# Performance work log

Hardware: AMD Instinct MI355X
Metric: run time of the kernel (lower is better)

## Reference

```python
import jax, jax.numpy as jnp
import numpy as np

N = 8192        # nodes
E = 262144      # edges (avg degree 32)
IN_CH = 256
CH = 128
SLOPE = 0.2     # PyG GATv2Conv default negative_slope


def gatv2(x, src, dst, wl, wr, att, b):
    """Single-head GATv2Conv (PyG defaults: share_weights=False, self-loops
    already appended to src/dst). x: [N, in]; wl, wr: [out, in]; att: [out]."""
    xl = x @ wl.T                      # [N, out] source-side transform (x_j)
    xr = x @ wr.T                      # [N, out] target-side transform (x_i)
    # per-edge attention logit: att . LeakyReLU(x_l[src] + x_r[dst])
    e = jax.nn.leaky_relu(xl[src] + xr[dst], SLOPE) @ att   # [E']
    # segment softmax over incoming edges of each target node
    m = jax.ops.segment_max(e, dst, num_segments=N)
    p = jnp.exp(e - m[dst])
    s = jax.ops.segment_sum(p, dst, num_segments=N)
    alpha = p / s[dst]                 # every node has a self-loop -> s > 0
    out = jax.ops.segment_sum(alpha[:, None] * xl[src], dst, num_segments=N)
    return out + b


def setup_inputs() -> dict:
    key = jax.random.key(0)
    ks = jax.random.split(key, 2 + 5 * 3)
    inp = {
        "x": jax.random.normal(ks[0], (N, IN_CH), dtype=jnp.float32),
        "edge_index": jax.random.randint(ks[1], (2, E), 0, N, dtype=jnp.int64),
    }
    dims = [(CH, IN_CH), (2 * CH, CH), (CH, 2 * CH), (CH, 2 * CH), (IN_CH, CH)]
    ki = 2
    for i, (oc, ic) in enumerate(dims, start=1):
        sc = (2.0 / (ic + oc)) ** 0.5  # glorot-ish
        inp[f"w{i}l"] = jax.random.normal(ks[ki], (oc, ic), dtype=jnp.float32) * sc
        inp[f"w{i}r"] = jax.random.normal(ks[ki + 1], (oc, ic), dtype=jnp.float32) * sc
        inp[f"a{i}"] = jax.random.normal(ks[ki + 2], (oc,), dtype=jnp.float32) * sc
        inp[f"b{i}"] = jnp.zeros((oc,), dtype=jnp.float32)
        ki += 3
    return inp


def reference(x, edge_index,
              w1l, w1r, a1, b1,
              w2l, w2r, a2, b2,
              w3l, w3r, a3, b3,
              w4l, w4r, a4, b4,
              w5l, w5r, a5, b5):
    loops = jnp.arange(N, dtype=edge_index.dtype)
    src = jnp.concatenate([edge_index[0], loops])   # add_self_loops=True
    dst = jnp.concatenate([edge_index[1], loops])
    h = jax.nn.relu(gatv2(x, src, dst, w1l, w1r, a1, b1))          # [N, CH]
    z = jax.nn.relu(gatv2(h, src, dst, w2l, w2r, a2, b2))          # [N, 2CH]
    re = jax.nn.relu(gatv2(z, src, dst, w3l, w3r, a3, b3))         # [N, CH]
    recon_edge = jax.nn.sigmoid(re @ re.T)                         # [N, N]
    xd = jax.nn.relu(gatv2(z, src, dst, w4l, w4r, a4, b4))         # [N, CH]
    x_rec = jax.nn.relu(gatv2(xd, src, dst, w5l, w5r, a5, b5))     # [N, IN_CH]
    return recon_edge, x_rec, z
```

## Files before the change

kernel.cpp:

```cpp
#include <hip/hip_runtime.h>
#include <hip/hip_bf16.h>
#include <math.h>

#define N_NODES 8192
#define N_EDGES 262144
#define EP (N_EDGES + N_NODES)
#define SLOPE 0.2f

typedef short bf16x8 __attribute__((ext_vector_type(8)));
typedef short short4v __attribute__((ext_vector_type(4)));
typedef float f32x4 __attribute__((ext_vector_type(4)));

__global__ void detect_i64(const int* __restrict__ raw, int* __restrict__ flag) {
    if (threadIdx.x == 0 && blockIdx.x == 0) {
        int acc = 0;
        for (int i = 0; i < 64; ++i) acc |= raw[2 * i + 1];
        *flag = (acc == 0) ? 1 : 0;
    }
}

__global__ void extract_hist(const int* __restrict__ raw, const int* __restrict__ flag,
                             int* __restrict__ esrc, int* __restrict__ edst,
                             int* __restrict__ counts) {
    int k = blockIdx.x * blockDim.x + threadIdx.x;
    if (k >= N_EDGES) return;
    int s, d;
    if (*flag) {
        s = raw[2 * (size_t)k];
        d = raw[2 * ((size_t)N_EDGES + k)];
    } else {
        s = raw[k];
        d = raw[N_EDGES + k];
    }
    esrc[k] = s;
    edst[k] = d;
    atomicAdd(&counts[d], 1);
}

__global__ void scan_k(const int* __restrict__ counts, int* __restrict__ row_ptr) {
    __shared__ int part[256];
    int t = threadIdx.x;
    int base = t * 32;
    int loc[32];
    int s = 0;
    for (int i = 0; i < 32; ++i) { loc[i] = s; s += counts[base + i] + 1; }
    part[t] = s;
    __syncthreads();
    for (int off = 1; off < 256; off <<= 1) {
        int tmp = (t >= off) ? part[t - off] : 0;
        __syncthreads();
        part[t] += tmp;
        __syncthreads();
    }
    int incl = part[t];
    int excl = incl - s;
    for (int i = 0; i < 32; ++i) row_ptr[base + i] = excl + loc[i];
    if (t == 255) row_ptr[N_NODES] = incl;
}

__global__ void scatter_k(const int* __restrict__ esrc, const int* __restrict__ edst,
                          const int* __restrict__ row_ptr, int* __restrict__ cursor,
                          int* __restrict__ ssrc) {
    int k = blockIdx.x * blockDim.x + threadIdx.x;
    if (k >= EP) return;
    int s, d;
    if (k < N_EDGES) { s = esrc[k]; d = edst[k]; }
    else             { s = d = k - N_EDGES; }
    int pos = row_ptr[d] + atomicAdd(&cursor[d], 1);
    ssrc[pos] = s;
}

__global__ void split3(const float* __restrict__ in, short* __restrict__ out, int logK) {
    int K = 1 << logK;
    int total = (N_NODES << logK) >> 2;
    int i = blockIdx.x * blockDim.x + threadIdx.x;
    if (i >= total) return;
    int r = i >> (logK - 2);
    int c4 = (i & ((1 << (logK - 2)) - 1)) << 2;
    f32x4 a = *(const f32x4*)&in[((size_t)r << logK) + c4];
    short4v h4, l4;
#pragma unroll
    for (int j = 0; j < 4; ++j) {
        __hip_bfloat16 hb = __float2bfloat16(a[j]);
        float hf = __bfloat162float(hb);
        __hip_bfloat16 lb = __float2bfloat16(a[j] - hf);
        h4[j] = *(short*)&hb;
        l4[j] = *(short*)&lb;
    }
    size_t ro = (size_t)r * (3 << logK);
    *(short4v*)&out[ro + c4] = h4;
    *(short4v*)&out[ro + K + c4] = l4;
    *(short4v*)&out[ro + 2 * K + c4] = h4;
}

struct WPrep {
    const float* wl[5];
    const float* wr[5];
    int oc[5];
    int lk[5];
};

__global__ void prep_w3_all(WPrep P, short* __restrict__ out) {
    int gid = blockIdx.x * blockDim.x + threadIdx.x;
    int l = gid >> 16;
    if (l >= 5) return;
    int rem = gid & 65535;
    int lk = P.lk[l], K = 1 << lk;
    int r = rem >> lk, c = rem & (K - 1);
    int OC = P.oc[l];
    const float* w = (r < OC) ? P.wl[l] : P.wr[l];
    int rr = (r < OC) ? r : r - OC;
    float a = w[((size_t)rr << lk) + c];
    __hip_bfloat16 hb = __float2bfloat16(a);
    float hf = __bfloat162float(hb);
    __hip_bfloat16 lb = __float2bfloat16(a - hf);
    short hs = *(short*)&hb, lo = *(short*)&lb;
    size_t ro = (size_t)l * 196608 + (size_t)r * 3 * K;
    out[ro + c] = hs;
    out[ro + K + c] = hs;
    out[ro + 2 * K + c] = lo;
}

#if __has_builtin(__builtin_amdgcn_global_load_lds)
#define GL16(gsrc, lbase, lofs)                                                       \
    __builtin_amdgcn_global_load_lds((const __attribute__((address_space(1))) void*)(gsrc), \
                                     (__attribute__((address_space(3))) void*)(lbase), 16, 0, 0)
#else
#define GL16(gsrc, lbase, lofs) (*(bf16x8*)((lbase) + (lofs)) = *(const bf16x8*)(gsrc))
#endif

__global__ __launch_bounds__(256) void gemm_bf16_nt(const short* __restrict__ A3,
                                                    const short* __restrict__ W3,
                                                    float* __restrict__ XL,
                                                    float* __restrict__ XR,
                                                    int K3, int N2, int OC) {
    __shared__ __align__(16) short As[2][4096];
    __shared__ __align__(16) short Bs[2][4096];
    int tid = threadIdx.x;
    int gx = gridDim.x;
    int lgx = (gx == 8) ? 3 : 2;
    int orig = blockIdx.x + (blockIdx.y << lgx);
    int nwg = gx << 7;
    int swzb = (orig & 7) * (nwg >> 3) + (orig >> 3);
    int bx = swzb & (gx - 1), by = swzb >> lgx;
    int i0 = by * 64, j0 = bx * 64;

    int wave = tid >> 6, lane = tid & 63;
    int b0 = wave * 1024 + lane * 16;
    int row0 = b0 >> 7;
    int rb0 = b0 & 127;
    int scb = rb0 ^ ((row0 & 7) << 4);
    const short* gA0 = A3 + (size_t)(i0 + row0) * K3 + (scb >> 1);
    const short* gA1 = A3 + (size_t)(i0 + row0 + 32) * K3 + (scb >> 1);
    const short* gB0 = W3 + (size_t)(j0 + row0) * K3 + (scb >> 1);
    const short* gB1 = W3 + (size_t)(j0 + row0 + 32) * K3 + (scb >> 1);
    int lofs = lane * 8;

#define STAGE(pb, k0s)                                      \
    do {                                                    \
        GL16(gA0 + (k0s), &As[pb][wave * 512], lofs);       \
        GL16(gA1 + (k0s), &As[pb][2048 + wave * 512], lofs);\
        GL16(gB0 + (k0s), &Bs[pb][wave * 512], lofs);       \
        GL16(gB1 + (k0s), &Bs[pb][2048 + wave * 512], lofs);\
    } while (0)

    int wr = (wave >> 1) * 32, wc = (wave & 1) * 32;
    int lm = lane & 15, quad = lane >> 4;
    f32x4 acc[2][2] = {};
    int nt = K3 >> 6;
    STAGE(0, 0);
    int cur = 0;
    for (int t = 0; t < nt; ++t) {
        if (t + 1 < nt) {
            STAGE(cur ^ 1, (t + 1) << 6);
            asm volatile("s_waitcnt vmcnt(4)" ::: "memory");
        } else {
            asm volatile("s_waitcnt vmcnt(0)" ::: "memory");
        }
        __builtin_amdgcn_s_barrier();
        __builtin_amdgcn_sched_barrier(0);
        const char* Ab = (const char*)&As[cur][0];
        const char* Bb = (const char*)&Bs[cur][0];
#pragma unroll
        for (int ks = 0; ks < 2; ++ks) {
            int kb = ks * 64 + quad * 16;
            bf16x8 a[2], b[2];
#pragma unroll
            for (int u = 0; u < 2; ++u) {
                int r = wr + u * 16 + lm;
                a[u] = *(const bf16x8*)(Ab + (((r << 7) | kb) ^ ((r & 7) << 4)));
            }
#pragma unroll
            for (int v = 0; v < 2; ++v) {
                int r = wc + v * 16 + lm;
                b[v] = *(const bf16x8*)(Bb + (((r << 7) | kb) ^ ((r & 7) << 4)));
            }
#pragma unroll
            for (int u = 0; u < 2; ++u)
#pragma unroll
                for (int v = 0; v < 2; ++v)
                    acc[u][v] = __builtin_amdgcn_mfma_f32_16x16x32_bf16(a[u], b[v], acc[u][v], 0, 0, 0);
        }
        __builtin_amdgcn_sched_barrier(0);
        __builtin_amdgcn_s_barrier();
        cur ^= 1;
    }
#undef STAGE
    float* Cb;
    int col0;
    if (j0 < OC) { Cb = XL; col0 = j0; } else { Cb = XR; col0 = j0 - OC; }
#pragma unroll
    for (int u = 0; u < 2; ++u)
#pragma unroll
        for (int v = 0; v < 2; ++v)
#pragma unroll
            for (int r = 0; r < 4; ++r) {
                int row = i0 + wr + u * 16 + quad * 4 + r;
                int col = col0 + wc + v * 16 + lm;
                Cb[(size_t)row * OC + col] = acc[u][v][r];
            }
}

#define LSTR 136

__global__ __launch_bounds__(256) void recon_mfma(const unsigned short* __restrict__ Rb,
                                                  float* __restrict__ C) {
    __shared__ __align__(16) short As[128 * LSTR];
    __shared__ __align__(16) short Bs[128 * LSTR];
    int tid = threadIdx.x;
    int orig = blockIdx.x + blockIdx.y * 64;
    int swzb = (orig & 7) * 512 + (orig >> 3);
    int bx = swzb & 63, by = swzb >> 6;
    int i0 = by * 128, j0 = bx * 128;
    const short* R = (const short*)Rb;
#pragma unroll
    for (int c = 0; c < 8; ++c) {
        int idx = tid + c * 256;
        int row = idx >> 4, col = (idx & 15) * 8;
        *(bf16x8*)(&As[row * LSTR + col]) = *(const bf16x8*)(&R[(size_t)(i0 + row) * 128 + col]);
        *(bf16x8*)(&Bs[row * LSTR + col]) = *(const bf16x8*)(&R[(size_t)(j0 + row) * 128 + col]);
    }
    __syncthreads();
    int wave = tid >> 6, lane = tid & 63;
    int wr = (wave >> 1) * 64, wc = (wave & 1) * 64;
    int lm = lane & 15, quad = lane >> 4;
    f32x4 acc[4][4] = {};
#pragma unroll
    for (int ks = 0; ks < 4; ++ks) {
        int ko = ks * 32 + quad * 8;
        bf16x8 a[4], b[4];
#pragma unroll
        for (int u = 0; u < 4; ++u)
            a[u] = *(const bf16x8*)(&As[(wr + u * 16 + lm) * LSTR + ko]);
#pragma unroll
        for (int v = 0; v < 4; ++v)
            b[v] = *(const bf16x8*)(&Bs[(wc + v * 16 + lm) * LSTR + ko]);
#pragma unroll
        for (int u = 0; u < 4; ++u)
#pragma unroll
            for (int v = 0; v < 4; ++v)
                acc[u][v] = __builtin_amdgcn_mfma_f32_16x16x32_bf16(a[u], b[v], acc[u][v], 0, 0, 0);
    }
#pragma unroll
    for (int u = 0; u < 4; ++u)
#pragma unroll
        for (int v = 0; v < 4; ++v)
#pragma unroll
            for (int r = 0; r < 4; ++r) {
                int row = i0 + wr + u * 16 + quad * 4 + r;
                int col = j0 + wc + v * 16 + lm;
                float val = acc[u][v][r];
                C[(size_t)row * 8192 + col] = 1.0f / (1.0f + __expf(-val));
            }
}

__global__ __launch_bounds__(256) void gat_node256(const int* __restrict__ row_ptr,
                                                   const int* __restrict__ ssrc,
                                                   const float* __restrict__ XL,
                                                   const float* __restrict__ XR,
                                                   const float* __restrict__ att,
                                                   const float* __restrict__ bias,
                                                   float* __restrict__ outf,
                                                   short* __restrict__ a3) {
    __shared__ float sacc[4][256];
    __shared__ float sm[4], ss[4];
    int d = blockIdx.x, t = threadIdx.x;
    int lane = t & 63, wave = t >> 6;
    int beg = row_ptr[d], end = row_ptr[d + 1];
    f32x4 xr = *(const f32x4*)&XR[(size_t)d * 256 + lane * 4];
    f32x4 at = *(const f32x4*)&att[lane * 4];
    float m = -INFINITY, s = 0.0f;
    f32x4 acc = {0.0f, 0.0f, 0.0f, 0.0f};
    for (int p = beg + wave; p < end; p += 4) {
        int si = ssrc[p];
        f32x4 v = *(const f32x4*)&XL[(size_t)si * 256 + lane * 4];
        float e = 0.0f;
#pragma unroll
        for (int j = 0; j < 4; ++j) {
            float u = v[j] + xr[j];
            u = (u > 0.0f) ? u : SLOPE * u;
            e += u * at[j];
        }
#pragma unroll
        for (int off = 32; off; off >>= 1) e += __shfl_xor(e, off, 64);
        float mn = fmaxf(m, e);
        float f = __expf(m - mn), p0 = __expf(e - mn);
        s = s * f + p0;
#pragma unroll
        for (int j = 0; j < 4; ++j) acc[j] = acc[j] * f + p0 * v[j];
        m = mn;
    }
    *(f32x4*)&sacc[wave][lane * 4] = acc;
    if (lane == 0) { sm[wave] = m; ss[wave] = s; }
    __syncthreads();
    float M = fmaxf(fmaxf(sm[0], sm[1]), fmaxf(sm[2], sm[3]));
    float tot = 0.0f, st = 0.0f;
#pragma unroll
    for (int w = 0; w < 4; ++w) {
        float fw = __expf(sm[w] - M);
        tot += sacc[w][t] * fw;
        st += ss[w] * fw;
    }
    float val = fmaxf(tot / st + bias[t], 0.0f);
    if (outf) outf[(size_t)d * 256 + t] = val;
    if (a3) {
        __hip_bfloat16 hb = __float2bfloat16(val);
        float hf = __bfloat162float(hb);
        __hip_bfloat16 lb = __float2bfloat16(val - hf);
        size_t ro = (size_t)d * 768;
        a3[ro + t] = *(short*)&hb;
        a3[ro + 256 + t] = *(short*)&lb;
        a3[ro + 512 + t] = *(short*)&hb;
    }
}

__global__ __launch_bounds__(256) void gat_node128(const int* __restrict__ row_ptr,
                                                   const int* __restrict__ ssrc,
                                                   const float* __restrict__ XL,
                                                   const float* __restrict__ XR,
                                                   const float* __restrict__ att,
                                                   const float* __restrict__ bias,
                                                   float* __restrict__ outf,
                                                   short* __restrict__ a3,
                                                   unsigned short* __restrict__ rb) {
    __shared__ float sacc[8][128];
    __shared__ float sm[8], ss[8];
    int d = blockIdx.x, t = threadIdx.x;
    int ln = t & 31, hw = t >> 5;
    int beg = row_ptr[d], end = row_ptr[d + 1];
    f32x4 xr = *(const f32x4*)&XR[(size_t)d * 128 + ln * 4];
    f32x4 at = *(const f32x4*)&att[ln * 4];
    float m = -INFINITY, s = 0.0f;
    f32x4 acc = {0.0f, 0.0f, 0.0f, 0.0f};
    for (int p = beg + hw; p < end; p += 8) {
        int si = ssrc[p];
        f32x4 v = *(const f32x4*)&XL[(size_t)si * 128 + ln * 4];
        float e = 0.0f;
#pragma unroll
        for (int j = 0; j < 4; ++j) {
            float u = v[j] + xr[j];
            u = (u > 0.0f) ? u : SLOPE * u;
            e += u * at[j];
        }
#pragma unroll
        for (int off = 16; off; off >>= 1) e += __shfl_xor(e, off, 32);
        float mn = fmaxf(m, e);
        float f = __expf(m - mn), p0 = __expf(e - mn);
        s = s * f + p0;
#pragma unroll
        for (int j = 0; j < 4; ++j) acc[j] = acc[j] * f + p0 * v[j];
        m = mn;
    }
    *(f32x4*)&sacc[hw][ln * 4] = acc;
    if (ln == 0) { sm[hw] = m; ss[hw] = s; }
    __syncthreads();
    if (t < 128) {
        float M = sm[0];
#pragma unroll
        for (int w = 1; w < 8; ++w) M = fmaxf(M, sm[w]);
        float tot = 0.0f, st = 0.0f;
#pragma unroll
        for (int w = 0; w < 8; ++w) {
            float fw = __expf(sm[w] - M);
            tot += sacc[w][t] * fw;
            st += ss[w] * fw;
        }
        float val = fmaxf(tot / st + bias[t], 0.0f);
        if (outf) outf[(size_t)d * 128 + t] = val;
        if (a3) {
            __hip_bfloat16 hb = __float2bfloat16(val);
            float hf = __bfloat162float(hb);
            __hip_bfloat16 lb = __float2bfloat16(val - hf);
            size_t ro = (size_t)d * 384;
            a3[ro + t] = *(short*)&hb;
            a3[ro + 128 + t] = *(short*)&lb;
            a3[ro + 256 + t] = *(short*)&hb;
        }
        if (rb) {
            __hip_bfloat16 hb = __float2bfloat16(val);
            rb[d * 128 + t] = *(unsigned short*)&hb;
        }
    }
}

static inline int ceil_div(int a, int b) { return (a + b - 1) / b; }

extern "C" void kernel_launch(void* const* d_in, const int* in_sizes, int n_in,
                              void* d_out, int out_size, void* d_ws, size_t ws_size,
                              hipStream_t stream) {
    const float* x    = (const float*)d_in[0];
    const int*   eraw = (const int*)d_in[1];

    WPrep P;
    const float* att[5];
    const float* bia[5];
    for (int l = 0; l < 5; ++l) {
        P.wl[l] = (const float*)d_in[2 + 4 * l + 0];
        P.wr[l] = (const float*)d_in[2 + 4 * l + 1];
        att[l]  = (const float*)d_in[2 + 4 * l + 2];
        bia[l]  = (const float*)d_in[2 + 4 * l + 3];
    }
    const int och[5]  = {128, 256, 128, 128, 256};
    const int logK[5] = {8, 7, 8, 8, 7};
    for (int l = 0; l < 5; ++l) { P.oc[l] = och[l]; P.lk[l] = logK[l]; }

    float* outp  = (float*)d_out;
    float* recon = outp;
    float* xrec  = outp + (size_t)67108864;
    float* zout  = outp + (size_t)69206016;

    float* W = (float*)d_ws;
    float* XL    = W;
    float* XR    = W + 2097152;
    short* A3    = (short*)(W + 4194304);
    short* W3all = (short*)(W + 7340032);
    unsigned short* Rb = (unsigned short*)(W + 7831552);
    int* I       = (int*)(W + 8355840);
    int* counts  = I;
    int* cursor  = I + 8192;
    int* row_ptr = I + 16384;
    int* ssrc    = I + 24577;
    int* esrc    = I + 294913;
    int* edst    = I + 557057;
    int* flag    = I + 819201;

    hipMemsetAsync(counts, 0, 2 * 8192 * sizeof(int), stream);
    detect_i64<<<1, 64, 0, stream>>>(eraw, flag);
    extract_hist<<<ceil_div(N_EDGES, 256), 256, 0, stream>>>(eraw, flag, esrc, edst, counts);
    scan_k<<<1, 256, 0, stream>>>(counts, row_ptr);
    scatter_k<<<ceil_div(EP, 256), 256, 0, stream>>>(esrc, edst, row_ptr, cursor, ssrc);

    prep_w3_all<<<1280, 256, 0, stream>>>(P, W3all);
    split3<<<ceil_div(N_NODES * 256 / 4, 256), 256, 0, stream>>>(x, A3, 8);

    for (int l = 0; l < 5; ++l) {
        int lk = logK[l], OC = och[l];
        int N2 = OC << 1, K3 = 3 << lk;

        dim3 g(N2 / 64, N_NODES / 64);
        gemm_bf16_nt<<<g, 256, 0, stream>>>(A3, W3all + (size_t)l * 196608, XL, XR, K3, N2, OC);

        if (OC == 128) {
            float* of = nullptr;
            short* a3 = (l == 0 || l == 3) ? A3 : nullptr;
            unsigned short* rb = (l == 2) ? Rb : nullptr;
            gat_node128<<<N_NODES, 256, 0, stream>>>(row_ptr, ssrc, XL, XR, att[l], bia[l], of, a3, rb);
        } else {
            float* of = (l == 1) ? zout : xrec;
            short* a3 = (l == 1) ? A3 : nullptr;
            gat_node256<<<N_NODES, 256, 0, stream>>>(row_ptr, ssrc, XL, XR, att[l], bia[l], of, a3);
        }

        if (l == 2) {
            dim3 gr(64, 64);
            recon_mfma<<<gr, 256, 0, stream>>>(Rb, recon);
        }
    }
}
```

Baseline: 596.2 us.

## Exploit recon symmetry, unroll GAT edge loops, fuse prep and detect kernels

The recon kernel now computes only upper-triangular 128x128 tiles (2080 blocks instead of 4096) and writes each off-diagonal tile twice, the second time transposed through LDS. This roughly halves the MFMA and sigmoid work while keeping the full 256MB output write. The GAT node kernels handle two edges per iteration to expose more memory-level parallelism. The int64 detection kernel is folded into extract_hist, and the x split and weight prep kernels are merged into one launch to cut launch overhead. The transposed write path adds LDS traffic and an extra sync.

```diff
diff --git a/kernel.cpp b/kernel.cpp
--- a/kernel.cpp
+++ b/kernel.cpp
@@ -11,21 +11,21 @@
 typedef short short4v __attribute__((ext_vector_type(4)));
 typedef float f32x4 __attribute__((ext_vector_type(4)));
 
-__global__ void detect_i64(const int* __restrict__ raw, int* __restrict__ flag) {
-    if (threadIdx.x == 0 && blockIdx.x == 0) {
-        int acc = 0;
-        for (int i = 0; i < 64; ++i) acc |= raw[2 * i + 1];
-        *flag = (acc == 0) ? 1 : 0;
-    }
-}
-
-__global__ void extract_hist(const int* __restrict__ raw, const int* __restrict__ flag,
+__global__ void extract_hist(const int* __restrict__ raw,
                              int* __restrict__ esrc, int* __restrict__ edst,
                              int* __restrict__ counts) {
-    int k = blockIdx.x * blockDim.x + threadIdx.x;
+    __shared__ int sflag;
+    int t = threadIdx.x;
+    if (t < 64) {
+        unsigned long long b = __ballot(raw[2 * t + 1] != 0);
+        if (t == 0) sflag = (b == 0ULL) ? 1 : 0;
+    }
+    __syncthreads();
+    int i64f = sflag;
+    int k = blockIdx.x * blockDim.x + t;
     if (k >= N_EDGES) return;
     int s, d;
-    if (*flag) {
+    if (i64f) {
         s = raw[2 * (size_t)k];
         d = raw[2 * ((size_t)N_EDGES + k)];
     } else {
@@ -70,29 +70,6 @@
     ssrc[pos] = s;
 }
 
-__global__ void split3(const float* __restrict__ in, short* __restrict__ out, int logK) {
-    int K = 1 << logK;
-    int total = (N_NODES << logK) >> 2;
-    int i = blockIdx.x * blockDim.x + threadIdx.x;
-    if (i >= total) return;
-    int r = i >> (logK - 2);
-    int c4 = (i & ((1 << (logK - 2)) - 1)) << 2;
-    f32x4 a = *(const f32x4*)&in[((size_t)r << logK) + c4];
-    short4v h4, l4;
-#pragma unroll
-    for (int j = 0; j < 4; ++j) {
-        __hip_bfloat16 hb = __float2bfloat16(a[j]);
-        float hf = __bfloat162float(hb);
-        __hip_bfloat16 lb = __float2bfloat16(a[j] - hf);
-        h4[j] = *(short*)&hb;
-        l4[j] = *(short*)&lb;
-    }
-    size_t ro = (size_t)r * (3 << logK);
-    *(short4v*)&out[ro + c4] = h4;
-    *(short4v*)&out[ro + K + c4] = l4;
-    *(short4v*)&out[ro + 2 * K + c4] = h4;
-}
-
 struct WPrep {
     const float* wl[5];
     const float* wr[5];
@@ -100,25 +77,45 @@
     int lk[5];
 };
 
-__global__ void prep_w3_all(WPrep P, short* __restrict__ out) {
+__global__ void prep_all(WPrep P, const float* __restrict__ x,
+                         short* __restrict__ W3all, short* __restrict__ A3) {
     int gid = blockIdx.x * blockDim.x + threadIdx.x;
-    int l = gid >> 16;
-    if (l >= 5) return;
-    int rem = gid & 65535;
-    int lk = P.lk[l], K = 1 << lk;
-    int r = rem >> lk, c = rem & (K - 1);
-    int OC = P.oc[l];
-    const float* w = (r < OC) ? P.wl[l] : P.wr[l];
-    int rr = (r < OC) ? r : r - OC;
-    float a = w[((size_t)rr << lk) + c];
-    __hip_bfloat16 hb = __float2bfloat16(a);
-    float hf = __bfloat162float(hb);
-    __hip_bfloat16 lb = __float2bfloat16(a - hf);
-    short hs = *(short*)&hb, lo = *(short*)&lb;
-    size_t ro = (size_t)l * 196608 + (size_t)r * 3 * K;
-    out[ro + c] = hs;
-    out[ro + K + c] = hs;
-    out[ro + 2 * K + c] = lo;
+    if (gid < 524288) {
+        int r = gid >> 6;
+        int c4 = (gid & 63) << 2;
+        f32x4 a = *(const f32x4*)&x[((size_t)r << 8) + c4];
+        short4v h4, l4;
+#pragma unroll
+        for (int j = 0; j < 4; ++j) {
+            __hip_bfloat16 hb = __float2bfloat16(a[j]);
+            float hf = __bfloat162float(hb);
+            __hip_bfloat16 lb = __float2bfloat16(a[j] - hf);
+            h4[j] = *(short*)&hb;
+            l4[j] = *(short*)&lb;
+        }
+        size_t ro = (size_t)r * 768;
+        *(short4v*)&A3[ro + c4] = h4;
+        *(short4v*)&A3[ro + 256 + c4] = l4;
+        *(short4v*)&A3[ro + 512 + c4] = h4;
+    } else {
+        int g = gid - 524288;
+        int l = g >> 16;
+        if (l >= 5) return;
+        int rem = g & 65535;
+        int lk = P.lk[l], K = 1 << lk;
+        int r = rem >> lk, c = rem & (K - 1);
+        int OC = P.oc[l];
+        const float* w = (r < OC) ? P.wl[l] : P.wr[l];
+        int rr = (r < OC) ? r : r - OC;
+        float a = w[((size_t)rr << lk) + c];
+        __hip_bfloat16 hb = __float2bfloat16(a);
+        float hf = __bfloat162float(hb);
+        __hip_bfloat16 lb = __float2bfloat16(a - hf);
+        size_t ro = (size_t)l * 196608 + (size_t)r * 3 * K;
+        W3all[ro + c] = *(short*)&hb;
+        W3all[ro + K + c] = *(short*)&hb;
+        W3all[ro + 2 * K + c] = *(short*)&lb;
+    }
 }
 
 #if __has_builtin(__builtin_amdgcn_global_load_lds)
@@ -223,15 +220,20 @@
 
 #define LSTR 136
 
-__global__ __launch_bounds__(256) void recon_mfma(const unsigned short* __restrict__ Rb,
-                                                  float* __restrict__ C) {
-    __shared__ __align__(16) short As[128 * LSTR];
-    __shared__ __align__(16) short Bs[128 * LSTR];
+__global__ __launch_bounds__(256) void recon_sym(const unsigned short* __restrict__ Rb,
+                                                 float* __restrict__ C) {
+    __shared__ __align__(16) short Sh[2 * 128 * LSTR];
+    short* As = Sh;
+    short* Bs = Sh + 128 * LSTR;
     int tid = threadIdx.x;
-    int orig = blockIdx.x + blockIdx.y * 64;
-    int swzb = (orig & 7) * 512 + (orig >> 3);
-    int bx = swzb & 63, by = swzb >> 6;
-    int i0 = by * 128, j0 = bx * 128;
+    int orig = blockIdx.x;
+    int s = (orig & 7) * 260 + (orig >> 3);
+    float ff = 64.5f - sqrtf(64.5f * 64.5f - 2.0f * (float)s);
+    int bi = (int)ff;
+    while (bi > 0 && 64 * bi - bi * (bi - 1) / 2 > s) --bi;
+    while (64 * (bi + 1) - (bi + 1) * bi / 2 <= s) ++bi;
+    int bj = bi + (s - (64 * bi - bi * (bi - 1) / 2));
+    int i0 = bi * 128, j0 = bj * 128;
     const short* R = (const short*)Rb;
 #pragma unroll
     for (int c = 0; c < 8; ++c) {
@@ -267,11 +269,29 @@
         for (int v = 0; v < 4; ++v)
 #pragma unroll
             for (int r = 0; r < 4; ++r) {
+                acc[u][v][r] = 1.0f / (1.0f + __expf(-acc[u][v][r]));
                 int row = i0 + wr + u * 16 + quad * 4 + r;
                 int col = j0 + wc + v * 16 + lm;
-                float val = acc[u][v][r];
-                C[(size_t)row * 8192 + col] = 1.0f / (1.0f + __expf(-val));
+                C[(size_t)row * 8192 + col] = acc[u][v][r];
             }
+    if (bi != bj) {
+        __syncthreads();
+        float* T = (float*)Sh;
+#pragma unroll
+        for (int u = 0; u < 4; ++u)
+#pragma unroll
+            for (int v = 0; v < 4; ++v)
+#pragma unroll
+                for (int r = 0; r < 4; ++r)
+                    T[(wr + u * 16 + quad * 4 + r) * 129 + (wc + v * 16 + lm)] = acc[u][v][r];
+        __syncthreads();
+#pragma unroll
+        for (int it = 0; it < 64; ++it) {
+            int idx = tid + it * 256;
+            int rp = idx >> 7, cp = idx & 127;
+            C[(size_t)(j0 + rp) * 8192 + (i0 + cp)] = T[cp * 129 + rp];
+        }
+    }
 }
 
 __global__ __launch_bounds__(256) void gat_node256(const int* __restrict__ row_ptr,
@@ -291,7 +311,30 @@
     f32x4 at = *(const f32x4*)&att[lane * 4];
     float m = -INFINITY, s = 0.0f;
     f32x4 acc = {0.0f, 0.0f, 0.0f, 0.0f};
-    for (int p = beg + wave; p < end; p += 4) {
+    int p = beg + wave;
+    for (; p + 4 < end; p += 8) {
+        int s0 = ssrc[p], s1 = ssrc[p + 4];
+        f32x4 v0 = *(const f32x4*)&XL[(size_t)s0 * 256 + lane * 4];
+        f32x4 v1 = *(const f32x4*)&XL[(size_t)s1 * 256 + lane * 4];
+        float e0 = 0.0f, e1 = 0.0f;
+#pragma unroll
+        for (int j = 0; j < 4; ++j) {
+            float u0 = v0[j] + xr[j]; u0 = (u0 > 0.0f) ? u0 : SLOPE * u0; e0 += u0 * at[j];
+            float u1 = v1[j] + xr[j]; u1 = (u1 > 0.0f) ? u1 : SLOPE * u1; e1 += u1 * at[j];
+        }
+#pragma unroll
+        for (int off = 32; off; off >>= 1) {
+            e0 += __shfl_xor(e0, off, 64);
+            e1 += __shfl_xor(e1, off, 64);
+        }
+        float mn = fmaxf(m, fmaxf(e0, e1));
+        float f = __expf(m - mn), q0 = __expf(e0 - mn), q1 = __expf(e1 - mn);
+        s = s * f + q0 + q1;
+#pragma unroll
+        for (int j = 0; j < 4; ++j) acc[j] = acc[j] * f + q0 * v0[j] + q1 * v1[j];
+        m = mn;
+    }
+    if (p < end) {
         int si = ssrc[p];
         f32x4 v = *(const f32x4*)&XL[(size_t)si * 256 + lane * 4];
         float e = 0.0f;
@@ -352,7 +395,30 @@
     f32x4 at = *(const f32x4*)&att[ln * 4];
     float m = -INFINITY, s = 0.0f;
     f32x4 acc = {0.0f, 0.0f, 0.0f, 0.0f};
-    for (int p = beg + hw; p < end; p += 8) {
+    int p = beg + hw;
+    for (; p + 8 < end; p += 16) {
+        int s0 = ssrc[p], s1 = ssrc[p + 8];
+        f32x4 v0 = *(const f32x4*)&XL[(size_t)s0 * 128 + ln * 4];
+        f32x4 v1 = *(const f32x4*)&XL[(size_t)s1 * 128 + ln * 4];
+        float e0 = 0.0f, e1 = 0.0f;
+#pragma unroll
+        for (int j = 0; j < 4; ++j) {
+            float u0 = v0[j] + xr[j]; u0 = (u0 > 0.0f) ? u0 : SLOPE * u0; e0 += u0 * at[j];
+            float u1 = v1[j] + xr[j]; u1 = (u1 > 0.0f) ? u1 : SLOPE * u1; e1 += u1 * at[j];
+        }
+#pragma unroll
+        for (int off = 16; off; off >>= 1) {
+            e0 += __shfl_xor(e0, off, 32);
+            e1 += __shfl_xor(e1, off, 32);
+        }
+        float mn = fmaxf(m, fmaxf(e0, e1));
+        float f = __expf(m - mn), q0 = __expf(e0 - mn), q1 = __expf(e1 - mn);
+        s = s * f + q0 + q1;
+#pragma unroll
+        for (int j = 0; j < 4; ++j) acc[j] = acc[j] * f + q0 * v0[j] + q1 * v1[j];
+        m = mn;
+    }
+    if (p < end) {
         int si = ssrc[p];
         f32x4 v = *(const f32x4*)&XL[(size_t)si * 128 + ln * 4];
         float e = 0.0f;
@@ -442,16 +508,13 @@
     int* ssrc    = I + 24577;
     int* esrc    = I + 294913;
     int* edst    = I + 557057;
-    int* flag    = I + 819201;
 
     hipMemsetAsync(counts, 0, 2 * 8192 * sizeof(int), stream);
-    detect_i64<<<1, 64, 0, stream>>>(eraw, flag);
-    extract_hist<<<ceil_div(N_EDGES, 256), 256, 0, stream>>>(eraw, flag, esrc, edst, counts);
+    extract_hist<<<ceil_div(N_EDGES, 256), 256, 0, stream>>>(eraw, esrc, edst, counts);
     scan_k<<<1, 256, 0, stream>>>(counts, row_ptr);
     scatter_k<<<ceil_div(EP, 256), 256, 0, stream>>>(esrc, edst, row_ptr, cursor, ssrc);
 
-    prep_w3_all<<<1280, 256, 0, stream>>>(P, W3all);
-    split3<<<ceil_div(N_NODES * 256 / 4, 256), 256, 0, stream>>>(x, A3, 8);
+    prep_all<<<3328, 256, 0, stream>>>(P, x, W3all, A3);
 
     for (int l = 0; l < 5; ++l) {
         int lk = logK[l], OC = och[l];
@@ -472,8 +535,7 @@
         }
 
         if (l == 2) {
-            dim3 gr(64, 64);
-            recon_mfma<<<gr, 256, 0, stream>>>(Rb, recon);
-        }
-    }
-}
+            recon_sym<<<2080, 256, 0, stream>>>(Rb, recon);
+        }
+    }
+}
```

After: 557.9 us. 1.07x faster.
